# Performance work log

Hardware: AMD Instinct MI355X
Metric: run time of the kernel (lower is better)

The kernel has to match this reference:

```python
import jax, jax.numpy as jnp
import numpy as np

N_PATCHES = 14
N_BLOCKS = 12
HIDDEN = 768
N_HEADS = 12
D_HEAD = HIDDEN // N_HEADS
MLP_RATIO = 4
OUT_D = 1000
BATCH = 32
C, H, W = 3, 224, 224
PS = H // N_PATCHES            # 16
INPUT_D = C * PS * PS          # 768
SEQ = N_PATCHES ** 2 + 1       # 197
LN_EPS = 1e-5


def _pos_emb(length, d):
    i = np.arange(length, dtype=np.float64)[:, None]
    j = np.arange(d, dtype=np.float64)[None, :]
    angle = i / (10000.0 ** ((j - (j % 2)) / d))
    pe = np.where(j % 2 == 0, np.sin(angle), np.cos(angle))
    return jnp.asarray(pe, dtype=jnp.float32)  # [length, d]


def setup_inputs() -> dict:
    key = jax.random.key(0)
    ks = jax.random.split(key, 16)
    s = 0.02
    inp = {
        "x": jax.random.normal(ks[0], (BATCH, C, H, W), jnp.float32),
        "W_map": jax.random.normal(ks[1], (INPUT_D, HIDDEN), jnp.float32) * s,
        "b_map": jnp.zeros((HIDDEN,), jnp.float32),
        "cls_tok": jax.random.uniform(ks[2], (1, HIDDEN), jnp.float32),
        "pos_emb": _pos_emb(SEQ, HIDDEN),
        "ln1_s": jnp.ones((N_BLOCKS, HIDDEN), jnp.float32),
        "ln1_b": jnp.zeros((N_BLOCKS, HIDDEN), jnp.float32),
        "Wq": jax.random.normal(ks[3], (N_BLOCKS, N_HEADS, D_HEAD, D_HEAD), jnp.float32) * s,
        "bq": jnp.zeros((N_BLOCKS, N_HEADS, D_HEAD), jnp.float32),
        "Wk": jax.random.normal(ks[4], (N_BLOCKS, N_HEADS, D_HEAD, D_HEAD), jnp.float32) * s,
        "bk": jnp.zeros((N_BLOCKS, N_HEADS, D_HEAD), jnp.float32),
        "Wv": jax.random.normal(ks[5], (N_BLOCKS, N_HEADS, D_HEAD, D_HEAD), jnp.float32) * s,
        "bv": jnp.zeros((N_BLOCKS, N_HEADS, D_HEAD), jnp.float32),
        "ln2_s": jnp.ones((N_BLOCKS, HIDDEN), jnp.float32),
        "ln2_b": jnp.zeros((N_BLOCKS, HIDDEN), jnp.float32),
        "W1": jax.random.normal(ks[6], (N_BLOCKS, HIDDEN, MLP_RATIO * HIDDEN), jnp.float32) * s,
        "b1": jnp.zeros((N_BLOCKS, MLP_RATIO * HIDDEN), jnp.float32),
        "W2": jax.random.normal(ks[7], (N_BLOCKS, MLP_RATIO * HIDDEN, HIDDEN), jnp.float32) * s,
        "b2": jnp.zeros((N_BLOCKS, HIDDEN), jnp.float32),
        "W_out": jax.random.normal(ks[8], (HIDDEN, OUT_D), jnp.float32) * s,
        "b_out": jnp.zeros((OUT_D,), jnp.float32),
    }
    return inp


def _layernorm(x, scale, bias):
    m = jnp.mean(x, axis=-1, keepdims=True)
    v = jnp.mean(jnp.square(x - m), axis=-1, keepdims=True)
    return (x - m) * jax.lax.rsqrt(v + LN_EPS) * scale + bias


def _patchify(x):
    # [N,C,H,W] -> [N, np*np, C*ps*ps], channel-major flatten per patch (matches torch flatten)
    n = x.shape[0]
    p = x.reshape(n, C, N_PATCHES, PS, N_PATCHES, PS)
    p = p.transpose(0, 2, 4, 1, 3, 5)  # [N, np, np, C, ps, ps]
    return p.reshape(n, N_PATCHES * N_PATCHES, INPUT_D)


def _msa(x, Wq, bq, Wk, bk, Wv, bv):
    # x: [N,S,D]; per-head separate linears, faithful scale = 1/sqrt(n_heads)
    n, s_, _ = x.shape
    xh = x.reshape(n, s_, N_HEADS, D_HEAD)
    q = jnp.einsum('nshd,hde->nhse', xh, Wq) + bq[None, :, None, :]
    k = jnp.einsum('nshd,hde->nhse', xh, Wk) + bk[None, :, None, :]
    v = jnp.einsum('nshd,hde->nhse', xh, Wv) + bv[None, :, None, :]
    scale = 1.0 / jnp.sqrt(jnp.float32(N_HEADS))
    att = jax.nn.softmax(jnp.einsum('nhse,nhte->nhst', q, k) * scale, axis=-1)
    o = jnp.einsum('nhst,nhte->nhse', att, v)
    return o.transpose(0, 2, 1, 3).reshape(n, s_, HIDDEN)


def reference(x, W_map, b_map, cls_tok, pos_emb, ln1_s, ln1_b, Wq, bq, Wk, bk, Wv, bv,
              ln2_s, ln2_b, W1, b1, W2, b2, W_out, b_out):
    n = x.shape[0]
    tokens = _patchify(x) @ W_map + b_map                       # [N, np^2, D]
    tokens = jnp.concatenate([jnp.broadcast_to(cls_tok[None], (n, 1, HIDDEN)), tokens], axis=1)
    h = tokens + pos_emb[None]                                  # [N, S, D]
    for blk in range(N_BLOCKS):
        attn_out = _msa(_layernorm(h, ln1_s[blk], ln1_b[blk]),
                        Wq[blk], bq[blk], Wk[blk], bk[blk], Wv[blk], bv[blk])
        out = h + attn_out
        # faithful to source: MLP branch reads norm2(x), not norm2(out)
        m = _layernorm(h, ln2_s[blk], ln2_b[blk])
        m = jax.nn.gelu(m @ W1[blk] + b1[blk], approximate=False) @ W2[blk] + b2[blk]
        h = out + m
    cls = h[:, 0]                                               # [N, D]
    return jax.nn.softmax(cls @ W_out + b_out, axis=1)          # [N, out_d]
```

## Files before the change

### kernel.cpp

```cpp
#include <hip/hip_runtime.h>
#include <math.h>

#define BATCH   32
#define SEQ     197
#define HIDDEN  768
#define NHEADS  12
#define DHEAD   64
#define NBLOCKS 12
#define MLP_D   3072
#define OUTD    1000
#define NPATCH  196
#define M_TOK   (BATCH*SEQ)
#define M_PAD   6400
#define LN_EPS  1e-5f
#define SP      208

typedef _Float16 f16;
typedef _Float16 f16x8 __attribute__((ext_vector_type(8)));
typedef _Float16 f16x4 __attribute__((ext_vector_type(4)));
typedef float    f32x4 __attribute__((ext_vector_type(4)));

__device__ __forceinline__ float gelu_exact(float x) {
    return 0.5f * x * (1.0f + erff(x * 0.70710678118654752f));
}

__device__ __forceinline__ void gload_lds16(const void* g, void* l) {
    __builtin_amdgcn_global_load_lds(
        (const __attribute__((address_space(1))) void*)g,
        (__attribute__((address_space(3))) void*)l, 16, 0, 0);
}

__device__ __forceinline__ f16x8 lds_ld(const char* base, int row, int rs, int kbyte) {
    return *(const f16x8*)(base + row*rs + (kbyte ^ ((row & 7) << 4)));
}

__device__ __forceinline__ f16x8 lds32(const char* buf, int row, int lg) {
    int p = row >> 1;
    int sl = (((row & 1) << 2) + lg) ^ (p & 7);
    return *(const f16x8*)(buf + p*128 + sl*16);
}

__global__ __launch_bounds__(256) void patchify_kernel(const float* __restrict__ x,
                                                       f16* __restrict__ patches) {
    int row = blockIdx.x;
    int n = row / NPATCH;
    int p = row % NPATCH;
    int pi = p / 14, pj = p % 14;
    for (int k = threadIdx.x; k < 768; k += 256) {
        int c   = k >> 8;
        int r   = (k >> 4) & 15;
        int col = k & 15;
        patches[(size_t)row*768 + k] =
            (f16)x[(((size_t)n*3 + c)*224 + (pi*16 + r))*224 + pj*16 + col];
    }
}

__global__ __launch_bounds__(256) void transT_kernel(const float* __restrict__ src,
                                                     f16* __restrict__ dst,
                                                     int R, int C) {
    const float* in = src + (size_t)blockIdx.z * R * C;
    f16* out = dst + (size_t)blockIdx.z * R * C;
    __shared__ float tile[64][65];
    int r0 = blockIdx.y * 64, c0 = blockIdx.x * 64;
    int t = threadIdx.x;
    int lr16 = t >> 4, lc4 = (t & 15) * 4;
    #pragma unroll
    for (int i = 0; i < 4; ++i) {
        int r = i*16 + lr16;
        float4 v = *(const float4*)&in[(size_t)(r0 + r)*C + c0 + lc4];
        tile[r][lc4] = v.x; tile[r][lc4+1] = v.y; tile[r][lc4+2] = v.z; tile[r][lc4+3] = v.w;
    }
    __syncthreads();
    #pragma unroll
    for (int i = 0; i < 4; ++i) {
        int c = i*16 + lr16;
        int r = lc4;
        f16x4 pv = { (f16)tile[r][c], (f16)tile[r+1][c], (f16)tile[r+2][c], (f16)tile[r+3][c] };
        *(f16x4*)&out[(size_t)(c0 + c)*R + r0 + r] = pv;
    }
}

__global__ __launch_bounds__(256) void convtrans2_kernel(const float* __restrict__ W1,
                                                         const float* __restrict__ W2,
                                                         f16* __restrict__ W1T,
                                                         f16* __restrict__ W2T) {
    int z = blockIdx.z;
    const float* in = z ? W2 : W1;
    f16* out = z ? W2T : W1T;
    int R = z ? MLP_D : HIDDEN;
    int C = z ? HIDDEN : MLP_D;
    int bx = z ? blockIdx.y : blockIdx.x;
    int by = z ? blockIdx.x : blockIdx.y;
    __shared__ float tile[32][33];
    int r0 = by * 32, c0 = bx * 32;
    int tx = threadIdx.x & 31, ty = threadIdx.x >> 5;
    #pragma unroll
    for (int i = 0; i < 4; ++i) {
        int r = ty + i*8;
        tile[r][tx] = in[(size_t)(r0 + r)*C + c0 + tx];
    }
    __syncthreads();
    #pragma unroll
    for (int i = 0; i < 4; ++i) {
        int r = ty + i*8;
        out[(size_t)(c0 + r)*R + r0 + tx] = (f16)tile[tx][r];
    }
}

__global__ __launch_bounds__(256) void qkvtrans_kernel(const float* __restrict__ Wq,
                                                       const float* __restrict__ Wk,
                                                       const float* __restrict__ Wv,
                                                       f16* __restrict__ outT) {
    int b = blockIdx.x;
    int blkL = b / 36, rem = b % 36;
    int hh = rem / 3, mat = rem % 3;
    const float* in = (mat == 0 ? Wq : mat == 1 ? Wk : Wv) + ((size_t)(blkL*12 + hh))*4096;
    f16* out = outT + (size_t)b * 4096;
    __shared__ float tile[64][65];
    int t = threadIdx.x;
    for (int i = t; i < 4096; i += 256) tile[i >> 6][i & 63] = in[i];
    __syncthreads();
    for (int i = t; i < 4096; i += 256) out[i] = (f16)tile[i & 63][i >> 6];
}

__global__ __launch_bounds__(256) void assemble_kernel(const float* __restrict__ tokens,
                                                       const float* __restrict__ cls,
                                                       const float* __restrict__ pos,
                                                       float* __restrict__ h) {
    int r = blockIdx.x;
    int n = r / SEQ, s = r % SEQ;
    for (int c = threadIdx.x; c < 768; c += 256) {
        float v = (s == 0) ? cls[c] : tokens[(size_t)(n*NPATCH + s - 1)*768 + c];
        h[(size_t)r*768 + c] = v + pos[s*768 + c];
    }
}

__global__ __launch_bounds__(256) void layernorm2_kernel(const float* __restrict__ x,
                                                         const float* __restrict__ s1,
                                                         const float* __restrict__ b1,
                                                         const float* __restrict__ s2,
                                                         const float* __restrict__ b2,
                                                         f16* __restrict__ o1,
                                                         f16* __restrict__ o2) {
    int r = blockIdx.x;
    int t = threadIdx.x;
    const float* xr = x + (size_t)r*768;
    float v0 = xr[t], v1 = xr[t+256], v2 = xr[t+512];
    float s = v0 + v1 + v2;
    #pragma unroll
    for (int off = 32; off > 0; off >>= 1) s += __shfl_xor(s, off);
    __shared__ float red[4];
    int wid = t >> 6, lane = t & 63;
    if (lane == 0) red[wid] = s;
    __syncthreads();
    float mean = (red[0]+red[1]+red[2]+red[3]) * (1.0f/768.0f);
    __syncthreads();
    float d0 = v0-mean, d1 = v1-mean, d2 = v2-mean;
    float q = d0*d0 + d1*d1 + d2*d2;
    #pragma unroll
    for (int off = 32; off > 0; off >>= 1) q += __shfl_xor(q, off);
    if (lane == 0) red[wid] = q;
    __syncthreads();
    float var = (red[0]+red[1]+red[2]+red[3]) * (1.0f/768.0f);
    float inv = rsqrtf(var + LN_EPS);
    d0 *= inv; d1 *= inv; d2 *= inv;
    f16* p1 = o1 + (size_t)r*768;
    f16* p2 = o2 + (size_t)r*768;
    p1[t]     = (f16)(d0*s1[t]     + b1[t]);
    p1[t+256] = (f16)(d1*s1[t+256] + b1[t+256]);
    p1[t+512] = (f16)(d2*s1[t+512] + b1[t+512]);
    p2[t]     = (f16)(d0*s2[t]     + b2[t]);
    p2[t+256] = (f16)(d1*s2[t+256] + b2[t+256]);
    p2[t+512] = (f16)(d2*s2[t+512] + b2[t+512]);
}

__global__ __launch_bounds__(256) void fused_attn_kernel(
        const f16* __restrict__ lnh, const f16* __restrict__ qkvT,
        const float* __restrict__ bq, const float* __restrict__ bk,
        const float* __restrict__ bv, float* __restrict__ O) {
    int n = blockIdx.x, h = blockIdx.y;
    int t = threadIdx.x, wid = t >> 6, lane = t & 63;
    int lr = lane & 15;
    int lg = lane >> 4;

    __shared__ char lds[145408];
    char* Xs  = lds;
    char* Qs  = lds + 26624;
    char* Ks  = lds + 53248;
    char* VsT = lds + 79872;
    char* Ws  = lds + 112640;
    char* Ps  = lds + 112640 + wid*8192;

    const char* xsrc = (const char*)(lnh + (size_t)n*SEQ*768 + h*64);
    for (int c = t; c < SP*8; c += 256) {
        int s = c >> 3, kb = (c & 7) * 16;
        f16x8 v = {};
        if (s < SEQ) v = *(const f16x8*)(xsrc + (size_t)s*1536 + kb);
        *(f16x8*)(Xs + s*128 + (kb ^ ((s & 7) << 4))) = v;
    }
    const char* wsrc = (const char*)(qkvT) + (size_t)h * 3 * 4096 * 2;
    for (int c = t; c < 1536; c += 256) {
        int byte = c * 16, row = byte >> 7, kb = byte & 127;
        f16x8 v = *(const f16x8*)(wsrc + byte);
        *(f16x8*)(Ws + row*128 + (kb ^ ((row & 7) << 4))) = v;
    }
    for (int c = t; c < 384; c += 256) {
        int e = c / 6, sl = c % 6;
        int kb = 416 + sl * 16;
        *(f16x8*)(VsT + e*512 + (kb ^ ((e & 7) << 4))) = (f16x8){};
    }
    __syncthreads();

    for (int idx = wid; idx < 39; idx += 4) {
        int mat = idx / 13, mt = idx % 13;
        const float* bias = (mat == 0) ? bq : (mat == 1) ? bk : bv;
        #pragma unroll
        for (int nt = 0; nt < 4; ++nt) {
            f32x4 acc = {};
            #pragma unroll
            for (int ks = 0; ks < 2; ++ks) {
                f16x8 a = lds_ld(Xs, mt*16 + lr, 128, lg*16 + ks*64);
                f16x8 b = lds_ld(Ws, mat*64 + nt*16 + lr, 128, lg*16 + ks*64);
                acc = __builtin_amdgcn_mfma_f32_16x16x32_f16(a, b, acc, 0, 0, 0);
            }
            float bb = bias[h*64 + nt*16 + lr];
            if (mat < 2) {
                char* dst = (mat == 0) ? Qs : Ks;
                #pragma unroll
                for (int j = 0; j < 4; ++j) {
                    int s = mt*16 + lg*4 + j;
                    int eb = (nt*16 + lr) * 2;
                    *(f16*)(dst + s*128 + (eb ^ ((s & 7) << 4))) = (f16)(acc[j] + bb);
                }
            } else {
                int e = nt*16 + lr;
                int sb = (mt*16 + lg*4) * 2;
                f16x4 pv;
                #pragma unroll
                for (int j = 0; j < 4; ++j) pv[j] = (f16)(acc[j] + bb);
                *(f16x4*)(VsT + e*512 + (sb ^ ((e & 7) << 4))) = pv;
            }
        }
    }
    __syncthreads();

    for (int c = lane; c < 96; c += 64) {
        int r = c / 6, kb = 416 + (c % 6) * 16;
        *(f16x8*)(Ps + r*512 + (kb ^ ((r & 7) << 4))) = (f16x8){};
    }

    const float scale = 0.28867513459481288f;
    for (int mt = wid; mt < 13; mt += 4) {
        f32x4 sacc[13];
        #pragma unroll
        for (int nt = 0; nt < 13; ++nt) sacc[nt] = (f32x4){};
        #pragma unroll
        for (int ks = 0; ks < 2; ++ks) {
            f16x8 a = lds_ld(Qs, mt*16 + lr, 128, lg*16 + ks*64);
            #pragma unroll
            for (int nt = 0; nt < 13; ++nt) {
                f16x8 b = lds_ld(Ks, nt*16 + lr, 128, lg*16 + ks*64);
                sacc[nt] = __builtin_amdgcn_mfma_f32_16x16x32_f16(a, b, sacc[nt], 0, 0, 0);
            }
        }
        float mx0 = -1e30f, mx1 = -1e30f, mx2 = -1e30f, mx3 = -1e30f;
        #pragma unroll
        for (int nt = 0; nt < 13; ++nt) {
            bool valid = (nt*16 + lr) < SEQ;
            #pragma unroll
            for (int j = 0; j < 4; ++j) {
                float v = valid ? sacc[nt][j] * scale : -1e30f;
                sacc[nt][j] = v;
            }
            mx0 = fmaxf(mx0, sacc[nt][0]); mx1 = fmaxf(mx1, sacc[nt][1]);
            mx2 = fmaxf(mx2, sacc[nt][2]); mx3 = fmaxf(mx3, sacc[nt][3]);
        }
        #pragma unroll
        for (int off = 1; off < 16; off <<= 1) {
            mx0 = fmaxf(mx0, __shfl_xor(mx0, off));
            mx1 = fmaxf(mx1, __shfl_xor(mx1, off));
            mx2 = fmaxf(mx2, __shfl_xor(mx2, off));
            mx3 = fmaxf(mx3, __shfl_xor(mx3, off));
        }
        float s0 = 0.f, s1 = 0.f, s2 = 0.f, s3 = 0.f;
        #pragma unroll
        for (int nt = 0; nt < 13; ++nt) {
            float p0 = expf(sacc[nt][0] - mx0); sacc[nt][0] = p0; s0 += p0;
            float p1 = expf(sacc[nt][1] - mx1); sacc[nt][1] = p1; s1 += p1;
            float p2 = expf(sacc[nt][2] - mx2); sacc[nt][2] = p2; s2 += p2;
            float p3 = expf(sacc[nt][3] - mx3); sacc[nt][3] = p3; s3 += p3;
        }
        #pragma unroll
        for (int off = 1; off < 16; off <<= 1) {
            s0 += __shfl_xor(s0, off); s1 += __shfl_xor(s1, off);
            s2 += __shfl_xor(s2, off); s3 += __shfl_xor(s3, off);
        }
        float i0 = 1.0f/s0, i1 = 1.0f/s1, i2 = 1.0f/s2, i3 = 1.0f/s3;
        #pragma unroll
        for (int nt = 0; nt < 13; ++nt) {
            int cb = (nt*16 + lr) * 2;
            { int r = lg*4 + 0; *(f16*)(Ps + r*512 + (cb ^ ((r & 7) << 4))) = (f16)(sacc[nt][0] * i0); }
            { int r = lg*4 + 1; *(f16*)(Ps + r*512 + (cb ^ ((r & 7) << 4))) = (f16)(sacc[nt][1] * i1); }
            { int r = lg*4 + 2; *(f16*)(Ps + r*512 + (cb ^ ((r & 7) << 4))) = (f16)(sacc[nt][2] * i2); }
            { int r = lg*4 + 3; *(f16*)(Ps + r*512 + (cb ^ ((r & 7) << 4))) = (f16)(sacc[nt][3] * i3); }
        }
        f32x4 oacc[4] = {};
        #pragma unroll
        for (int ks = 0; ks < 8; ++ks) {
            f16x8 a = lds_ld(Ps, lr, 512, lg*16 + ks*64);
            #pragma unroll
            for (int nt = 0; nt < 4; ++nt) {
                f16x8 b = lds_ld(VsT, nt*16 + lr, 512, lg*16 + ks*64);
                oacc[nt] = __builtin_amdgcn_mfma_f32_16x16x32_f16(a, b, oacc[nt], 0, 0, 0);
            }
        }
        #pragma unroll
        for (int nt = 0; nt < 4; ++nt) {
            #pragma unroll
            for (int j = 0; j < 4; ++j) {
                int s = mt*16 + lg*4 + j;
                if (s < SEQ)
                    O[((size_t)(n*SEQ + s))*768 + h*64 + nt*16 + lr] = oacc[nt][j];
            }
        }
    }
}

template<int MODE, int TN>
__global__ __launch_bounds__(256) void hgemm_kernel(
        const f16* __restrict__ A,
        const f16* __restrict__ BT,
        const float* __restrict__ bias,
        const float* __restrict__ res1,
        const float* __restrict__ res2,
        void* __restrict__ Cout, int M, int N, int K, int nbx) {
    constexpr int BISS = TN / 64;
    constexpr int WN   = TN / 2;
    constexpr int NFR  = WN / 16;
    __shared__ f16 As[2][128*32];
    __shared__ f16 Bs[2][TN*32];
    int t = threadIdx.x;
    int wid = t >> 6, lane = t & 63;
    int lr = lane & 15, lg = lane >> 4;
    int wr = wid >> 1, wc = wid & 1;

    int nwg = gridDim.x, bid = blockIdx.x;
    int q = nwg >> 3, r = nwg & 7;
    int xcd = bid & 7, idx = bid >> 3;
    int swz = (xcd < r) ? xcd*(q+1) + idx : r*(q+1) + (xcd-r)*q + idx;
    int bn = (swz % nbx) * TN;
    int bm = (swz / nbx) * 128;

    int agrow[2], agk[2], bgrow[BISS], bgk[BISS];
    #pragma unroll
    for (int i = 0; i < 2; ++i) {
        int fb = i*4096 + wid*1024 + lane*16;
        int p = fb >> 7, u = ((fb >> 4) & 7) ^ (p & 7);
        agrow[i] = 2*p + (u >> 2); agk[i] = (u & 3) * 8;
    }
    #pragma unroll
    for (int i = 0; i < BISS; ++i) {
        int fb = i*4096 + wid*1024 + lane*16;
        int p = fb >> 7, u = ((fb >> 4) & 7) ^ (p & 7);
        bgrow[i] = 2*p + (u >> 2); bgk[i] = (u & 3) * 8;
    }

    #define STAGE(P, K0)                                                          \
        do {                                                                      \
            _Pragma("unroll")                                                     \
            for (int i = 0; i < 2; ++i)                                           \
                gload_lds16(A + (size_t)(bm + agrow[i])*K + (K0) + agk[i],        \
                            (char*)&As[P][0] + i*4096 + wid*1024);                \
            _Pragma("unroll")                                                     \
            for (int i = 0; i < BISS; ++i)                                        \
                gload_lds16(BT + (size_t)(bn + bgrow[i])*K + (K0) + bgk[i],       \
                            (char*)&Bs[P][0] + i*4096 + wid*1024);                \
        } while (0)

    f32x4 acc[4][NFR] = {};
    int nk = K >> 5;

    STAGE(0, 0);
    __syncthreads();
    for (int kt = 0; kt < nk; ++kt) {
        int cur = kt & 1;
        if (kt + 1 < nk) STAGE(cur ^ 1, (kt + 1) * 32);
        const char* Ab = (const char*)&As[cur][0];
        const char* Bb = (const char*)&Bs[cur][0];
        f16x8 a[4], b[NFR];
        #pragma unroll
        for (int m = 0; m < 4; ++m)
            a[m] = lds32(Ab, wr*64 + m*16 + lr, lg);
        #pragma unroll
        for (int nn = 0; nn < NFR; ++nn)
            b[nn] = lds32(Bb, wc*WN + nn*16 + lr, lg);
        #pragma unroll
        for (int m = 0; m < 4; ++m)
            #pragma unroll
            for (int nn = 0; nn < NFR; ++nn)
                acc[m][nn] = __builtin_amdgcn_mfma_f32_16x16x32_f16(a[m], b[nn], acc[m][nn], 0, 0, 0);
        __syncthreads();
    }
    #undef STAGE

    int row0 = bm + wr*64 + lg*4;
    int col0 = bn + wc*WN + lr;
    #pragma unroll
    for (int m = 0; m < 4; ++m) {
        #pragma unroll
        for (int nn = 0; nn < NFR; ++nn) {
            int col = col0 + nn*16;
            float bv = bias[col];
            #pragma unroll
            for (int j = 0; j < 4; ++j) {
                int row = row0 + m*16 + j;
                if (row >= M) continue;
                float v = acc[m][nn][j] + bv;
                size_t idx = (size_t)row*N + col;
                if (MODE == 0) {
                    if (res1) v += res1[idx] + res2[idx];
                    ((float*)Cout)[idx] = v;
                } else {
                    ((f16*)Cout)[idx] = (f16)gelu_exact(v);
                }
            }
        }
    }
}

__global__ __launch_bounds__(256) void head_kernel(const float* __restrict__ h,
                                                   const float* __restrict__ W_out,
                                                   const float* __restrict__ b_out,
                                                   float* __restrict__ out) {
    int n = blockIdx.x, t = threadIdx.x;
    __shared__ float xs[HIDDEN];
    __shared__ float red[4];
    const float* hr = h + (size_t)n*SEQ*HIDDEN;
    for (int k = t; k < HIDDEN; k += 256) xs[k] = hr[k];
    __syncthreads();

    bool v3 = t < (OUTD - 768);
    int c3 = v3 ? (t + 768) : t;
    float a0 = 0.f, a1 = 0.f, a2 = 0.f, a3 = 0.f;
    #pragma unroll 8
    for (int k = 0; k < HIDDEN; ++k) {
        float xv = xs[k];
        const float* wr = W_out + (size_t)k*OUTD;
        a0 = fmaf(xv, wr[t],       a0);
        a1 = fmaf(xv, wr[t + 256], a1);
        a2 = fmaf(xv, wr[t + 512], a2);
        a3 = fmaf(xv, wr[c3],      a3);
    }
    a0 += b_out[t]; a1 += b_out[t + 256]; a2 += b_out[t + 512];
    a3 = v3 ? (a3 + b_out[t + 768]) : -1e30f;

    int wid = t >> 6, lane = t & 63;
    float mx = fmaxf(fmaxf(a0, a1), fmaxf(a2, a3));
    #pragma unroll
    for (int off = 32; off > 0; off >>= 1) mx = fmaxf(mx, __shfl_xor(mx, off));
    if (lane == 0) red[wid] = mx;
    __syncthreads();
    mx = fmaxf(fmaxf(red[0], red[1]), fmaxf(red[2], red[3]));
    __syncthreads();

    float p0 = expf(a0 - mx), p1 = expf(a1 - mx), p2 = expf(a2 - mx);
    float p3 = v3 ? expf(a3 - mx) : 0.f;
    float s = p0 + p1 + p2 + p3;
    #pragma unroll
    for (int off = 32; off > 0; off >>= 1) s += __shfl_xor(s, off);
    if (lane == 0) red[wid] = s;
    __syncthreads();
    s = red[0] + red[1] + red[2] + red[3];
    float inv = 1.0f / s;

    float* orow = out + (size_t)n*OUTD;
    orow[t]       = p0 * inv;
    orow[t + 256] = p1 * inv;
    orow[t + 512] = p2 * inv;
    if (v3) orow[t + 768] = p3 * inv;
}

extern "C" void kernel_launch(void* const* d_in, const int* in_sizes, int n_in,
                              void* d_out, int out_size, void* d_ws, size_t ws_size,
                              hipStream_t stream) {
    const float* x     = (const float*)d_in[0];
    const float* W_map = (const float*)d_in[1];
    const float* b_map = (const float*)d_in[2];
    const float* cls_t = (const float*)d_in[3];
    const float* pos   = (const float*)d_in[4];
    const float* ln1_s = (const float*)d_in[5];
    const float* ln1_b = (const float*)d_in[6];
    const float* Wq    = (const float*)d_in[7];
    const float* bq    = (const float*)d_in[8];
    const float* Wk    = (const float*)d_in[9];
    const float* bk    = (const float*)d_in[10];
    const float* Wv    = (const float*)d_in[11];
    const float* bv    = (const float*)d_in[12];
    const float* ln2_s = (const float*)d_in[13];
    const float* ln2_b = (const float*)d_in[14];
    const float* W1    = (const float*)d_in[15];
    const float* b1    = (const float*)d_in[16];
    const float* W2    = (const float*)d_in[17];
    const float* b2    = (const float*)d_in[18];
    const float* W_out = (const float*)d_in[19];
    const float* b_out = (const float*)d_in[20];
    float* out = (float*)d_out;

    const size_t LAYER_W = (size_t)HIDDEN * MLP_D;

    char* w = (char*)d_ws;
    const size_t SZ32 = (size_t)M_TOK * HIDDEN * 4;
    float* h        = (float*)w;  w += SZ32;
    float* attn_out = (float*)w;  w += SZ32;
    f16*   mid_h    = (f16*)w;    w += (size_t)M_PAD * MLP_D * 2;
    f16*   lnh1     = (f16*)w;    w += (size_t)M_PAD * HIDDEN * 2;
    f16*   lnh2     = (f16*)w;    w += (size_t)M_PAD * HIDDEN * 2;
    f16*   WmapT    = (f16*)w;    w += (size_t)768 * 768 * 2;
    f16*   qkvT     = (f16*)w;    w += (size_t)NBLOCKS * NHEADS * 3 * 64 * 64 * 2;
    size_t base_used = (size_t)(w - (char*)d_ws);
    bool big = ws_size >= base_used + 2 * NBLOCKS * LAYER_W * 2;
    f16* W1T = (f16*)w;  w += (big ? NBLOCKS : 1) * LAYER_W * 2;
    f16* W2T = (f16*)w;  w += (big ? NBLOCKS : 1) * LAYER_W * 2;

    f16* patches_h = mid_h;
    patchify_kernel<<<BATCH*NPATCH, 256, 0, stream>>>(x, patches_h);
    {
        dim3 g(12, 12, 1);
        transT_kernel<<<g, 256, 0, stream>>>(W_map, WmapT, 768, 768);
    }
    qkvtrans_kernel<<<NBLOCKS*NHEADS*3, 256, 0, stream>>>(Wq, Wk, Wv, qkvT);
    if (big) {
        dim3 g1(MLP_D/64, HIDDEN/64, NBLOCKS);
        transT_kernel<<<g1, 256, 0, stream>>>(W1, W1T, HIDDEN, MLP_D);
        dim3 g2(HIDDEN/64, MLP_D/64, NBLOCKS);
        transT_kernel<<<g2, 256, 0, stream>>>(W2, W2T, MLP_D, HIDDEN);
    }
    hgemm_kernel<0,64><<<49*12, 256, 0, stream>>>(patches_h, WmapT, b_map,
                                                  nullptr, nullptr,
                                                  (void*)attn_out, BATCH*NPATCH, 768, 768, 12);
    assemble_kernel<<<M_TOK, 256, 0, stream>>>(attn_out, cls_t, pos, h);

    for (int blk = 0; blk < NBLOCKS; ++blk) {
        f16* w1t = big ? (W1T + (size_t)blk * LAYER_W) : W1T;
        f16* w2t = big ? (W2T + (size_t)blk * LAYER_W) : W2T;
        layernorm2_kernel<<<M_TOK, 256, 0, stream>>>(h,
            ln1_s + blk*768, ln1_b + blk*768, ln2_s + blk*768, ln2_b + blk*768,
            lnh1, lnh2);
        if (!big) {
            dim3 g(MLP_D/32, HIDDEN/32, 2);
            convtrans2_kernel<<<g, 256, 0, stream>>>(W1 + (size_t)blk*LAYER_W,
                                                     W2 + (size_t)blk*LAYER_W, w1t, w2t);
        }
        {
            dim3 g(BATCH, NHEADS);
            fused_attn_kernel<<<g, 256, 0, stream>>>(lnh1,
                qkvT + (size_t)blk*NHEADS*3*4096,
                bq + (size_t)blk*768, bk + (size_t)blk*768, bv + (size_t)blk*768,
                attn_out);
        }
        hgemm_kernel<1,128><<<50*24, 256, 0, stream>>>(lnh2, w1t, b1 + (size_t)blk*MLP_D,
                                                       nullptr, nullptr,
                                                       (void*)mid_h, M_TOK, MLP_D, 768, 24);
        hgemm_kernel<0,64><<<50*12, 256, 0, stream>>>(mid_h, w2t, b2 + (size_t)blk*HIDDEN,
                                                      h, attn_out,
                                                      (void*)h, M_TOK, HIDDEN, MLP_D, 12);
    }

    head_kernel<<<BATCH, 256, 0, stream>>>(h, W_out, b_out, out);
}
```

Before: 2.678 ms.

## Use wave-per-row layernorm, 512-thread attention blocks, narrower MLP1 tiles

Layernorm now handles one row per 64-lane wave with float4 loads and f16x4 stores. This removes the shared-memory reductions and block barriers, and the launch has a quarter as many blocks. The fused attention kernel moves to 512 threads (8 waves) and places the extra per-wave P buffers in Xs space and an enlarged LDS region, so Q/K/V projection and score tiles spread across more waves. The first MLP GEMM switches to a 64-wide N tile with twice as many blocks. These trade more parallelism and occupancy against extra LDS use, and risk Ps overwriting Xs while other waves may still be reading it.

```diff
diff --git a/kernel.cpp b/kernel.cpp
--- a/kernel.cpp
+++ b/kernel.cpp
@@ -142,39 +142,44 @@
                                                          const float* __restrict__ b2,
                                                          f16* __restrict__ o1,
                                                          f16* __restrict__ o2) {
-    int r = blockIdx.x;
-    int t = threadIdx.x;
-    const float* xr = x + (size_t)r*768;
-    float v0 = xr[t], v1 = xr[t+256], v2 = xr[t+512];
-    float s = v0 + v1 + v2;
+    int wid = threadIdx.x >> 6, lane = threadIdx.x & 63;
+    int r = blockIdx.x * 4 + wid;
+    const float4* xr = (const float4*)(x + (size_t)r * 768);
+    float4 v[3];
+    v[0] = xr[lane]; v[1] = xr[lane + 64]; v[2] = xr[lane + 128];
+    float s = v[0].x+v[0].y+v[0].z+v[0].w + v[1].x+v[1].y+v[1].z+v[1].w
+            + v[2].x+v[2].y+v[2].z+v[2].w;
     #pragma unroll
     for (int off = 32; off > 0; off >>= 1) s += __shfl_xor(s, off);
-    __shared__ float red[4];
-    int wid = t >> 6, lane = t & 63;
-    if (lane == 0) red[wid] = s;
-    __syncthreads();
-    float mean = (red[0]+red[1]+red[2]+red[3]) * (1.0f/768.0f);
-    __syncthreads();
-    float d0 = v0-mean, d1 = v1-mean, d2 = v2-mean;
-    float q = d0*d0 + d1*d1 + d2*d2;
+    float mean = s * (1.0f/768.0f);
+    float q = 0.f;
+    #pragma unroll
+    for (int j = 0; j < 3; ++j) {
+        float a = v[j].x-mean, b = v[j].y-mean, c = v[j].z-mean, d = v[j].w-mean;
+        q += a*a + b*b + c*c + d*d;
+    }
     #pragma unroll
     for (int off = 32; off > 0; off >>= 1) q += __shfl_xor(q, off);
-    if (lane == 0) red[wid] = q;
-    __syncthreads();
-    float var = (red[0]+red[1]+red[2]+red[3]) * (1.0f/768.0f);
-    float inv = rsqrtf(var + LN_EPS);
-    d0 *= inv; d1 *= inv; d2 *= inv;
-    f16* p1 = o1 + (size_t)r*768;
-    f16* p2 = o2 + (size_t)r*768;
-    p1[t]     = (f16)(d0*s1[t]     + b1[t]);
-    p1[t+256] = (f16)(d1*s1[t+256] + b1[t+256]);
-    p1[t+512] = (f16)(d2*s1[t+512] + b1[t+512]);
-    p2[t]     = (f16)(d0*s2[t]     + b2[t]);
-    p2[t+256] = (f16)(d1*s2[t+256] + b2[t+256]);
-    p2[t+512] = (f16)(d2*s2[t+512] + b2[t+512]);
-}
-
-__global__ __launch_bounds__(256) void fused_attn_kernel(
+    float inv = rsqrtf(q * (1.0f/768.0f) + LN_EPS);
+    #pragma unroll
+    for (int j = 0; j < 3; ++j) {
+        int col = (lane + 64*j) * 4;
+        float4 sc1 = *(const float4*)(s1 + col);
+        float4 bb1 = *(const float4*)(b1 + col);
+        float4 sc2 = *(const float4*)(s2 + col);
+        float4 bb2 = *(const float4*)(b2 + col);
+        float a = (v[j].x-mean)*inv, b = (v[j].y-mean)*inv,
+              c = (v[j].z-mean)*inv, d = (v[j].w-mean)*inv;
+        f16x4 w1 = { (f16)(a*sc1.x+bb1.x), (f16)(b*sc1.y+bb1.y),
+                     (f16)(c*sc1.z+bb1.z), (f16)(d*sc1.w+bb1.w) };
+        f16x4 w2 = { (f16)(a*sc2.x+bb2.x), (f16)(b*sc2.y+bb2.y),
+                     (f16)(c*sc2.z+bb2.z), (f16)(d*sc2.w+bb2.w) };
+        *(f16x4*)(o1 + (size_t)r*768 + col) = w1;
+        *(f16x4*)(o2 + (size_t)r*768 + col) = w2;
+    }
+}
+
+__global__ __launch_bounds__(512) void fused_attn_kernel(
         const f16* __restrict__ lnh, const f16* __restrict__ qkvT,
         const float* __restrict__ bq, const float* __restrict__ bk,
         const float* __restrict__ bv, float* __restrict__ O) {
@@ -183,35 +188,37 @@
     int lr = lane & 15;
     int lg = lane >> 4;
 
-    __shared__ char lds[145408];
+    __shared__ char lds[153600];
     char* Xs  = lds;
     char* Qs  = lds + 26624;
     char* Ks  = lds + 53248;
     char* VsT = lds + 79872;
     char* Ws  = lds + 112640;
-    char* Ps  = lds + 112640 + wid*8192;
+    char* Ps  = (wid < 3) ? (lds + wid*8192)
+              : (wid < 6) ? (lds + 112640 + (wid-3)*8192)
+                          : (lds + 137216 + (wid-6)*8192);
 
     const char* xsrc = (const char*)(lnh + (size_t)n*SEQ*768 + h*64);
-    for (int c = t; c < SP*8; c += 256) {
+    for (int c = t; c < SP*8; c += 512) {
         int s = c >> 3, kb = (c & 7) * 16;
         f16x8 v = {};
         if (s < SEQ) v = *(const f16x8*)(xsrc + (size_t)s*1536 + kb);
         *(f16x8*)(Xs + s*128 + (kb ^ ((s & 7) << 4))) = v;
     }
     const char* wsrc = (const char*)(qkvT) + (size_t)h * 3 * 4096 * 2;
-    for (int c = t; c < 1536; c += 256) {
+    for (int c = t; c < 1536; c += 512) {
         int byte = c * 16, row = byte >> 7, kb = byte & 127;
         f16x8 v = *(const f16x8*)(wsrc + byte);
         *(f16x8*)(Ws + row*128 + (kb ^ ((row & 7) << 4))) = v;
     }
-    for (int c = t; c < 384; c += 256) {
+    for (int c = t; c < 384; c += 512) {
         int e = c / 6, sl = c % 6;
         int kb = 416 + sl * 16;
         *(f16x8*)(VsT + e*512 + (kb ^ ((e & 7) << 4))) = (f16x8){};
     }
     __syncthreads();
 
-    for (int idx = wid; idx < 39; idx += 4) {
+    for (int idx = wid; idx < 39; idx += 8) {
         int mat = idx / 13, mt = idx % 13;
         const float* bias = (mat == 0) ? bq : (mat == 1) ? bk : bv;
         #pragma unroll
@@ -250,7 +257,7 @@
     }
 
     const float scale = 0.28867513459481288f;
-    for (int mt = wid; mt < 13; mt += 4) {
+    for (int mt = wid; mt < 13; mt += 8) {
         f32x4 sacc[13];
         #pragma unroll
         for (int nt = 0; nt < 13; ++nt) sacc[nt] = (f32x4){};
@@ -543,7 +550,7 @@
     for (int blk = 0; blk < NBLOCKS; ++blk) {
         f16* w1t = big ? (W1T + (size_t)blk * LAYER_W) : W1T;
         f16* w2t = big ? (W2T + (size_t)blk * LAYER_W) : W2T;
-        layernorm2_kernel<<<M_TOK, 256, 0, stream>>>(h,
+        layernorm2_kernel<<<M_TOK/4, 256, 0, stream>>>(h,
             ln1_s + blk*768, ln1_b + blk*768, ln2_s + blk*768, ln2_b + blk*768,
             lnh1, lnh2);
         if (!big) {
@@ -553,14 +560,14 @@
         }
         {
             dim3 g(BATCH, NHEADS);
-            fused_attn_kernel<<<g, 256, 0, stream>>>(lnh1,
+            fused_attn_kernel<<<g, 512, 0, stream>>>(lnh1,
                 qkvT + (size_t)blk*NHEADS*3*4096,
                 bq + (size_t)blk*768, bk + (size_t)blk*768, bv + (size_t)blk*768,
                 attn_out);
         }
-        hgemm_kernel<1,128><<<50*24, 256, 0, stream>>>(lnh2, w1t, b1 + (size_t)blk*MLP_D,
-                                                       nullptr, nullptr,
-                                                       (void*)mid_h, M_TOK, MLP_D, 768, 24);
+        hgemm_kernel<1,64><<<50*48, 256, 0, stream>>>(lnh2, w1t, b1 + (size_t)blk*MLP_D,
+                                                      nullptr, nullptr,
+                                                      (void*)mid_h, M_TOK, MLP_D, 768, 48);
         hgemm_kernel<0,64><<<50*12, 256, 0, stream>>>(mid_h, w2t, b2 + (size_t)blk*HIDDEN,
                                                       h, attn_out,
                                                       (void*)h, M_TOK, HIDDEN, MLP_D, 12);
```

Measured after the change: 2.344 ms. -12.5%, faster.
